# Kernel optimization log

Hardware: AMD Instinct MI355X
Metric: run time of the kernel (lower is better)

## Reference

```python
import jax, jax.numpy as jnp
import numpy as np

N = 50000      # nodes
K = 15         # k_max candidate neighbors per node
D = 128        # node_dim
H = 64         # hidden_dim
K_MIN = 2.0
K_MAX = 15.0
TAU = 0.5      # edge_tau
LAM = 1.0      # selector_lambda


def setup_inputs() -> dict:
    key = jax.random.key(0)
    ks = jax.random.split(key, 16)
    x = jax.random.normal(ks[0], (N, D), dtype=jnp.float32)
    src = jax.random.randint(ks[1], (N * K,), 0, N)
    dst = jnp.repeat(jnp.arange(N), K)  # edges grouped by dst, as the module requires
    edge_index = jnp.stack([src, dst]).astype(jnp.int64)
    edge_dist = jax.random.uniform(ks[2], (N * K,), dtype=jnp.float32)

    def lin(k, fin, fout):
        return jax.random.normal(k, (fin, fout), dtype=jnp.float32) / np.sqrt(fin)

    EIN = 2 * D + 1  # edge MLP input: [x_dst, x_src, dist]
    return {
        "x": x, "edge_index": edge_index, "edge_dist": edge_dist,
        "ew1": lin(ks[3], EIN, H), "eb1": jnp.zeros((H,), jnp.float32),
        "ew2": lin(ks[4], H, H),   "eb2": jnp.zeros((H,), jnp.float32),
        "ew3": lin(ks[5], H, 1),   "eb3": jnp.zeros((1,), jnp.float32),
        "dw1": lin(ks[6], D + 1, H), "db1": jnp.zeros((H,), jnp.float32),
        "dw2": lin(ks[7], H, H),     "db2": jnp.zeros((H,), jnp.float32),
        "dw3": lin(ks[8], H, 1),     "db3": jnp.zeros((1,), jnp.float32),
    }


def reference(x, edge_index, edge_dist, ew1, eb1, ew2, eb2, ew3, eb3,
              dw1, db1, dw2, db2, dw3, db3):
    src_mat = edge_index[0].reshape(N, K)              # (N, K)
    x_src = x[src_mat]                                 # gather: (N, K, D)
    x_dst = jnp.broadcast_to(x[:, None, :], (N, K, D))
    edge_feat = jnp.concatenate([x_dst, x_src, edge_dist.reshape(N, K, 1)], axis=-1)

    # edge MLP -> logits (eval mode: no gumbel-logistic noise)
    h = jax.nn.relu(edge_feat @ ew1 + eb1)
    h = jax.nn.relu(h @ ew2 + eb2)
    edge_logits = (h @ ew3 + eb3)[..., 0]              # (N, K)
    edge_energy = jax.nn.sigmoid(edge_logits / TAU)

    # degree MLP -> continuous k per node
    degree_hint = edge_energy.sum(axis=1, keepdims=True)
    g = jax.nn.relu(jnp.concatenate([x, degree_hint], axis=1) @ dw1 + db1)
    g = jax.nn.relu(g @ dw2 + db2)
    k_raw = (g @ dw3 + db3)[:, 0]
    k_cont = K_MIN + (K_MAX - K_MIN) * jax.nn.sigmoid(k_raw)  # (N,)

    # per-node descending sort + straight-through top-k gate
    perm = jnp.argsort(-edge_energy, axis=1)
    energy_sorted = jnp.take_along_axis(edge_energy, perm, axis=1)
    ranks = jnp.arange(1, K + 1, dtype=x.dtype)[None, :]
    gate_soft = jax.nn.sigmoid((k_cont[:, None] - ranks) / LAM)
    k_int = jnp.clip(jnp.round(k_cont), K_MIN, K_MAX)
    gate_hard = (ranks <= k_int[:, None]).astype(gate_soft.dtype)
    gate = gate_soft + jax.lax.stop_gradient(gate_hard - gate_soft)

    gated_sorted = energy_sorted * gate
    inv_perm = jnp.argsort(perm, axis=1)               # undo the sort
    edge_gate = jnp.take_along_axis(gate, inv_perm, axis=1)
    edge_weight = jnp.take_along_axis(gated_sorted, inv_perm, axis=1)

    denom = jnp.maximum(edge_weight.sum(axis=1, keepdims=True), 1e-12)
    edge_weight = edge_weight / denom
    return (edge_weight.reshape(-1), edge_gate.reshape(-1),
            edge_energy.reshape(-1), k_cont)
```

## Files before the change

kernel.cpp:

```cpp
#include <hip/hip_runtime.h>
#include <cmath>

#define NN 50000
#define KK 15
#define DD 128
#define HH 64
#define NKE (NN * KK)
#define TOFF ((size_t)DD * NN)
#define WS_NEED ((TOFF + 3 * (size_t)NN * HH) * 4)

__global__ __launch_bounds__(256) void kT(const float* __restrict__ x,
                                          float* __restrict__ xT) {
    __shared__ float s[64][DD + 1];
    int t = threadIdx.x;
    int r0 = blockIdx.x * 64;
#pragma unroll
    for (int i = 0; i < 8; ++i) {
        int idx = i * 256 + t;
        int rr = idx >> 5, cc = idx & 31;
        if (r0 + rr < NN) {
            float4 v = *(const float4*)(x + (size_t)(r0 + rr) * DD + cc * 4);
            s[rr][cc * 4 + 0] = v.x; s[rr][cc * 4 + 1] = v.y;
            s[rr][cc * 4 + 2] = v.z; s[rr][cc * 4 + 3] = v.w;
        }
    }
    __syncthreads();
    int lane = t & 63, wq = t >> 6;
    int n = r0 + lane;
    if (n >= NN) return;
#pragma unroll
    for (int i = 0; i < 32; ++i) {
        int k = i * 4 + wq;
        xT[(size_t)k * NN + n] = s[lane][k];
    }
}

__global__ __launch_bounds__(128, 4) void kP2(const float* __restrict__ xT,
                                              const float* __restrict__ ew1,
                                              const float* __restrict__ dw1,
                                              float* __restrict__ xabc) {
    int seg = blockIdx.y;
    const float* W = (seg == 0) ? ew1 : (seg == 1) ? (ew1 + DD * HH) : dw1;
    float* o = xabc + (size_t)seg * NN * HH;
    int n = blockIdx.x * 128 + threadIdx.x;
    if (n >= NN) return;

    float acc[HH];
#pragma unroll
    for (int j = 0; j < HH; ++j) acc[j] = 0.f;

#pragma unroll 1
    for (int k4 = 0; k4 < DD / 4; ++k4) {
        float x0 = xT[(size_t)(k4 * 4 + 0) * NN + n];
        float x1 = xT[(size_t)(k4 * 4 + 1) * NN + n];
        float x2 = xT[(size_t)(k4 * 4 + 2) * NN + n];
        float x3 = xT[(size_t)(k4 * 4 + 3) * NN + n];
        float xv[4] = {x0, x1, x2, x3};
#pragma unroll
        for (int m = 0; m < 4; ++m) {
            const float* wr = W + (k4 * 4 + m) * HH;
#pragma unroll
            for (int j4 = 0; j4 < 16; ++j4) {
                float4 w = *(const float4*)(wr + j4 * 4);
                acc[j4 * 4 + 0] = fmaf(xv[m], w.x, acc[j4 * 4 + 0]);
                acc[j4 * 4 + 1] = fmaf(xv[m], w.y, acc[j4 * 4 + 1]);
                acc[j4 * 4 + 2] = fmaf(xv[m], w.z, acc[j4 * 4 + 2]);
                acc[j4 * 4 + 3] = fmaf(xv[m], w.w, acc[j4 * 4 + 3]);
            }
        }
    }
    float* orow = o + (size_t)n * HH;
#pragma unroll
    for (int j4 = 0; j4 < 16; ++j4) {
        float4 v;
        v.x = acc[j4 * 4 + 0]; v.y = acc[j4 * 4 + 1];
        v.z = acc[j4 * 4 + 2]; v.w = acc[j4 * 4 + 3];
        *(float4*)(orow + j4 * 4) = v;
    }
}

__global__ __launch_bounds__(256, 4) void kP_fb(const float* __restrict__ x,
                                                const float* __restrict__ ew1,
                                                const float* __restrict__ dw1,
                                                float* __restrict__ xabc) {
    int lane = threadIdx.x & 63;
    int wv = threadIdx.x >> 6;
    int r0 = blockIdx.x * 32 + wv * 8;
    if (r0 >= NN) return;
    const float* W0 = ew1;
    const float* W1 = ew1 + DD * HH;
    const float* W2 = dw1;
    const float* xw = x + (size_t)r0 * DD;
    float a0[8], a1[8], a2[8];
#pragma unroll
    for (int r = 0; r < 8; ++r) { a0[r] = 0.f; a1[r] = 0.f; a2[r] = 0.f; }
#pragma unroll 1
    for (int i4 = 0; i4 < DD / 4; ++i4) {
        float w00 = W0[(i4 * 4 + 0) * HH + lane];
        float w01 = W0[(i4 * 4 + 1) * HH + lane];
        float w02 = W0[(i4 * 4 + 2) * HH + lane];
        float w03 = W0[(i4 * 4 + 3) * HH + lane];
        float w10 = W1[(i4 * 4 + 0) * HH + lane];
        float w11 = W1[(i4 * 4 + 1) * HH + lane];
        float w12 = W1[(i4 * 4 + 2) * HH + lane];
        float w13 = W1[(i4 * 4 + 3) * HH + lane];
        float w20 = W2[(i4 * 4 + 0) * HH + lane];
        float w21 = W2[(i4 * 4 + 1) * HH + lane];
        float w22 = W2[(i4 * 4 + 2) * HH + lane];
        float w23 = W2[(i4 * 4 + 3) * HH + lane];
#pragma unroll
        for (int r = 0; r < 8; ++r) {
            float4 xv = *(const float4*)(xw + r * DD + i4 * 4);
            a0[r] = fmaf(xv.x, w00, a0[r]); a0[r] = fmaf(xv.y, w01, a0[r]);
            a0[r] = fmaf(xv.z, w02, a0[r]); a0[r] = fmaf(xv.w, w03, a0[r]);
            a1[r] = fmaf(xv.x, w10, a1[r]); a1[r] = fmaf(xv.y, w11, a1[r]);
            a1[r] = fmaf(xv.z, w12, a1[r]); a1[r] = fmaf(xv.w, w13, a1[r]);
            a2[r] = fmaf(xv.x, w20, a2[r]); a2[r] = fmaf(xv.y, w21, a2[r]);
            a2[r] = fmaf(xv.z, w22, a2[r]); a2[r] = fmaf(xv.w, w23, a2[r]);
        }
    }
    float* o0 = xabc + (size_t)r0 * HH + lane;
    float* o1 = xabc + (size_t)NN * HH + (size_t)r0 * HH + lane;
    float* o2 = xabc + 2 * (size_t)NN * HH + (size_t)r0 * HH + lane;
#pragma unroll
    for (int r = 0; r < 8; ++r) {
        o0[r * HH] = a0[r]; o1[r * HH] = a1[r]; o2[r * HH] = a2[r];
    }
}

__global__ __launch_bounds__(128, 4) void kE(const int* __restrict__ srcIdx,
                                             const float* __restrict__ dist,
                                             const float* __restrict__ xabc,
                                             const float* __restrict__ ew1,
                                             const float* __restrict__ eb1,
                                             const float* __restrict__ ew2,
                                             const float* __restrict__ eb2,
                                             const float* __restrict__ ew3,
                                             const float* __restrict__ eb3,
                                             float* __restrict__ energy_out) {
    int e = blockIdx.x * 128 + threadIdx.x;
    if (e >= NKE) return;
    int s = srcIdx[e];
    int d = e / KK;
    float dd = dist[e];
    const float* A = xabc + (size_t)d * HH;
    const float* B = xabc + (size_t)NN * HH + (size_t)s * HH;
    const float* w1l = ew1 + 2 * DD * HH;

    float acc[HH];
#pragma unroll
    for (int j = 0; j < HH; ++j) acc[j] = 0.f;

    float4 a4 = *(const float4*)A;
    float4 bp0 = *(const float4*)B;
    float4 bp1 = *(const float4*)(B + 4);
#pragma unroll 1
    for (int i4 = 0; i4 < HH / 4; ++i4) {
        float4 a = a4, b = bp0;
        int n1 = (i4 + 1 < 16) ? (i4 + 1) : 15;
        int n2 = (i4 + 2 < 16) ? (i4 + 2) : 15;
        a4 = *(const float4*)(A + n1 * 4);
        bp0 = bp1;
        bp1 = *(const float4*)(B + n2 * 4);
        float h[4];
        h[0] = fmaxf(a.x + b.x + dd * w1l[i4 * 4 + 0] + eb1[i4 * 4 + 0], 0.f);
        h[1] = fmaxf(a.y + b.y + dd * w1l[i4 * 4 + 1] + eb1[i4 * 4 + 1], 0.f);
        h[2] = fmaxf(a.z + b.z + dd * w1l[i4 * 4 + 2] + eb1[i4 * 4 + 2], 0.f);
        h[3] = fmaxf(a.w + b.w + dd * w1l[i4 * 4 + 3] + eb1[i4 * 4 + 3], 0.f);
#pragma unroll
        for (int k = 0; k < 4; ++k) {
            const float* wr = ew2 + (i4 * 4 + k) * HH;
#pragma unroll
            for (int j4 = 0; j4 < 16; ++j4) {
                float4 w = *(const float4*)(wr + j4 * 4);
                acc[j4 * 4 + 0] = fmaf(h[k], w.x, acc[j4 * 4 + 0]);
                acc[j4 * 4 + 1] = fmaf(h[k], w.y, acc[j4 * 4 + 1]);
                acc[j4 * 4 + 2] = fmaf(h[k], w.z, acc[j4 * 4 + 2]);
                acc[j4 * 4 + 3] = fmaf(h[k], w.w, acc[j4 * 4 + 3]);
            }
        }
    }
    float lg = eb3[0];
#pragma unroll
    for (int j = 0; j < HH; ++j)
        lg = fmaf(fmaxf(acc[j] + eb2[j], 0.f), ew3[j], lg);
    energy_out[e] = 1.f / (1.f + expf(-2.f * lg));
}

__global__ __launch_bounds__(128, 4) void kF(const float* __restrict__ xabc,
                                             const float* __restrict__ dw1,
                                             const float* __restrict__ db1,
                                             const float* __restrict__ dw2,
                                             const float* __restrict__ db2,
                                             const float* __restrict__ dw3,
                                             const float* __restrict__ db3,
                                             float* __restrict__ out) {
    int n = blockIdx.x * 128 + threadIdx.x;
    if (n >= NN) return;
    const float* energy = out + 2 * (size_t)NKE;

    float ev[KK];
    float dh = 0.f;
#pragma unroll
    for (int j = 0; j < KK; ++j) {
        ev[j] = energy[(size_t)n * KK + j];
        dh += ev[j];
    }

    const float* XC = xabc + 2 * (size_t)NN * HH + (size_t)n * HH;
    const float* w1l = dw1 + DD * HH;

    float acc[HH];
#pragma unroll
    for (int j = 0; j < HH; ++j) acc[j] = 0.f;

    float4 c4 = *(const float4*)XC;
#pragma unroll 1
    for (int i4 = 0; i4 < HH / 4; ++i4) {
        float4 c = c4;
        int nx = (i4 + 1 < 16) ? (i4 + 1) : 15;
        c4 = *(const float4*)(XC + nx * 4);
        float cv[4] = {c.x, c.y, c.z, c.w};
#pragma unroll
        for (int m = 0; m < 4; ++m) {
            int k = i4 * 4 + m;
            float g = fmaxf(cv[m] + dh * w1l[k] + db1[k], 0.f);
            const float* wr = dw2 + k * HH;
#pragma unroll
            for (int j4 = 0; j4 < 16; ++j4) {
                float4 w = *(const float4*)(wr + j4 * 4);
                acc[j4 * 4 + 0] = fmaf(g, w.x, acc[j4 * 4 + 0]);
                acc[j4 * 4 + 1] = fmaf(g, w.y, acc[j4 * 4 + 1]);
                acc[j4 * 4 + 2] = fmaf(g, w.z, acc[j4 * 4 + 2]);
                acc[j4 * 4 + 3] = fmaf(g, w.w, acc[j4 * 4 + 3]);
            }
        }
    }
    float kraw = db3[0];
#pragma unroll
    for (int j = 0; j < HH; ++j)
        kraw = fmaf(fmaxf(acc[j] + db2[j], 0.f), dw3[j], kraw);

    float kcont = 2.f + 13.f / (1.f + expf(-kraw));
    out[3 * (size_t)NKE + n] = kcont;

    float se[16];
    int si[16];
#pragma unroll
    for (int j = 0; j < KK; ++j) { se[j] = ev[j]; si[j] = j; }
    se[15] = -1.f; si[15] = 15;

#pragma unroll
    for (int p = 1; p < 16; p <<= 1) {
#pragma unroll
        for (int k = p; k >= 1; k >>= 1) {
#pragma unroll
            for (int j = k & (p - 1); j + k < 16; j += 2 * k) {
#pragma unroll
                for (int i = 0; i < k; ++i) {
                    int a = i + j, b = i + j + k;
                    if (b < 16 && (a / (2 * p)) == (b / (2 * p))) {
                        bool sw = (se[b] > se[a]) ||
                                  (se[b] == se[a] && si[b] < si[a]);
                        float ea = sw ? se[b] : se[a];
                        float eb = sw ? se[a] : se[b];
                        int ia = sw ? si[b] : si[a];
                        int ib = sw ? si[a] : si[b];
                        se[a] = ea; se[b] = eb; si[a] = ia; si[b] = ib;
                    }
                }
            }
        }
    }

    float kint = rintf(kcont);
    kint = fminf(fmaxf(kint, 2.f), 15.f);

    float wsrt[KK];
    float denom = 0.f;
#pragma unroll
    for (int r = 0; r < KK; ++r) {
        float sel = ((float)(r + 1) <= kint) ? 1.f : 0.f;
        float wvv = se[r] * sel;
        wsrt[r] = wvv;
        denom += wvv;
    }
    denom = fmaxf(denom, 1e-12f);

#pragma unroll
    for (int r = 0; r < KK; ++r) {
        float sel = ((float)(r + 1) <= kint) ? 1.f : 0.f;
        int j0 = si[r];
        out[(size_t)NKE + (size_t)n * KK + j0] = sel;
        out[(size_t)n * KK + j0] = wsrt[r] / denom;
    }
}

extern "C" void kernel_launch(void* const* d_in, const int* in_sizes, int n_in,
                              void* d_out, int out_size, void* d_ws, size_t ws_size,
                              hipStream_t stream) {
    const float* x   = (const float*)d_in[0];
    const int*   ei  = (const int*)d_in[1];
    const float* ed  = (const float*)d_in[2];
    const float* ew1 = (const float*)d_in[3];
    const float* eb1 = (const float*)d_in[4];
    const float* ew2 = (const float*)d_in[5];
    const float* eb2 = (const float*)d_in[6];
    const float* ew3 = (const float*)d_in[7];
    const float* eb3 = (const float*)d_in[8];
    const float* dw1 = (const float*)d_in[9];
    const float* db1 = (const float*)d_in[10];
    const float* dw2 = (const float*)d_in[11];
    const float* db2 = (const float*)d_in[12];
    const float* dw3 = (const float*)d_in[13];
    const float* db3 = (const float*)d_in[14];
    float* out = (float*)d_out;
    float* ws  = (float*)d_ws;

    bool big = (ws_size >= WS_NEED);
    float* xabc = big ? (ws + TOFF) : ws;

    if (big) {
        hipLaunchKernelGGL(kT, dim3((NN + 63) / 64), dim3(256), 0, stream, x, ws);
        hipLaunchKernelGGL(kP2, dim3((NN + 127) / 128, 3), dim3(128), 0, stream,
                           ws, ew1, dw1, xabc);
    } else {
        hipLaunchKernelGGL(kP_fb, dim3((NN + 31) / 32), dim3(256), 0, stream,
                           x, ew1, dw1, xabc);
    }
    hipLaunchKernelGGL(kE, dim3((NKE + 127) / 128), dim3(128), 0, stream,
                       ei, ed, xabc, ew1, eb1, ew2, eb2, ew3, eb3,
                       out + 2 * (size_t)NKE);
    hipLaunchKernelGGL(kF, dim3((NN + 127) / 128), dim3(128), 0, stream,
                       xabc, dw1, db1, dw2, db2, dw3, db3, out);
}
```

Baseline: 326.9 us.

## Fuse edge MLP with degree MLP and split K across threads in projection

The edge-energy kernel and the per-node degree/sort kernel are merged into one kernel with 960-thread blocks. Each block handles 64 nodes' edges, keeps the energies in shared memory, and then lets 64 threads run the degree MLP, sort and gating. The projection kernel now splits the 128-long reduction across two thread halves and combines the partial sums in shared memory, doubling the threads available. This saves a launch and the energy re-read, but the node phase runs only one wavefront per large block, leaving most of that block idle. The 960-thread blocks with launch_bounds(960,4) may also force register spills for the 64-float accumulators.

```diff
diff --git a/kernel.cpp b/kernel.cpp
--- a/kernel.cpp
+++ b/kernel.cpp
@@ -35,47 +35,233 @@
     }
 }
 
-__global__ __launch_bounds__(128, 4) void kP2(const float* __restrict__ xT,
+__global__ __launch_bounds__(256, 4) void kP4(const float* __restrict__ xT,
                                               const float* __restrict__ ew1,
                                               const float* __restrict__ dw1,
                                               float* __restrict__ xabc) {
+    __shared__ float comb[HH * 128];
     int seg = blockIdx.y;
     const float* W = (seg == 0) ? ew1 : (seg == 1) ? (ew1 + DD * HH) : dw1;
-    float* o = xabc + (size_t)seg * NN * HH;
-    int n = blockIdx.x * 128 + threadIdx.x;
+    int t = threadIdx.x;
+    int nloc = t & 127;
+    int kh = t >> 7;
+    int n = blockIdx.x * 128 + nloc;
+    bool active = (n < NN);
+
+    float acc[HH];
+#pragma unroll
+    for (int j = 0; j < HH; ++j) acc[j] = 0.f;
+
+    if (active) {
+#pragma unroll 1
+        for (int k4 = kh * 16; k4 < kh * 16 + 16; ++k4) {
+            float x0 = xT[(size_t)(k4 * 4 + 0) * NN + n];
+            float x1 = xT[(size_t)(k4 * 4 + 1) * NN + n];
+            float x2 = xT[(size_t)(k4 * 4 + 2) * NN + n];
+            float x3 = xT[(size_t)(k4 * 4 + 3) * NN + n];
+            float xv[4] = {x0, x1, x2, x3};
+#pragma unroll
+            for (int m = 0; m < 4; ++m) {
+                const float* wr = W + (k4 * 4 + m) * HH;
+#pragma unroll
+                for (int j4 = 0; j4 < 16; ++j4) {
+                    float4 w = *(const float4*)(wr + j4 * 4);
+                    acc[j4 * 4 + 0] = fmaf(xv[m], w.x, acc[j4 * 4 + 0]);
+                    acc[j4 * 4 + 1] = fmaf(xv[m], w.y, acc[j4 * 4 + 1]);
+                    acc[j4 * 4 + 2] = fmaf(xv[m], w.z, acc[j4 * 4 + 2]);
+                    acc[j4 * 4 + 3] = fmaf(xv[m], w.w, acc[j4 * 4 + 3]);
+                }
+            }
+        }
+    }
+    if (kh == 1) {
+#pragma unroll
+        for (int j = 0; j < HH; ++j) comb[j * 128 + nloc] = acc[j];
+    }
+    __syncthreads();
+    if (kh == 0 && active) {
+#pragma unroll
+        for (int j = 0; j < HH; ++j) acc[j] += comb[j * 128 + nloc];
+        float* orow = xabc + (size_t)seg * NN * HH + (size_t)n * HH;
+#pragma unroll
+        for (int j4 = 0; j4 < 16; ++j4) {
+            float4 v;
+            v.x = acc[j4 * 4 + 0]; v.y = acc[j4 * 4 + 1];
+            v.z = acc[j4 * 4 + 2]; v.w = acc[j4 * 4 + 3];
+            *(float4*)(orow + j4 * 4) = v;
+        }
+    }
+}
+
+__global__ __launch_bounds__(960, 4) void kEF(const int* __restrict__ srcIdx,
+                                              const float* __restrict__ dist,
+                                              const float* __restrict__ xabc,
+                                              const float* __restrict__ ew1,
+                                              const float* __restrict__ eb1,
+                                              const float* __restrict__ ew2,
+                                              const float* __restrict__ eb2,
+                                              const float* __restrict__ ew3,
+                                              const float* __restrict__ eb3,
+                                              const float* __restrict__ dw1,
+                                              const float* __restrict__ db1,
+                                              const float* __restrict__ dw2,
+                                              const float* __restrict__ db2,
+                                              const float* __restrict__ dw3,
+                                              const float* __restrict__ db3,
+                                              float* __restrict__ out) {
+    __shared__ float ebuf[960];
+    int e = blockIdx.x * 960 + threadIdx.x;
+    float* energy_out = out + 2 * (size_t)NKE;
+
+    if (e < NKE) {
+        int s = srcIdx[e];
+        int d = e / KK;
+        float dd = dist[e];
+        const float* A = xabc + (size_t)d * HH;
+        const float* B = xabc + (size_t)NN * HH + (size_t)s * HH;
+        const float* w1l = ew1 + 2 * DD * HH;
+
+        float acc[HH];
+#pragma unroll
+        for (int j = 0; j < HH; ++j) acc[j] = 0.f;
+
+        float4 a4 = *(const float4*)A;
+        float4 bp0 = *(const float4*)B;
+        float4 bp1 = *(const float4*)(B + 4);
+#pragma unroll 1
+        for (int i4 = 0; i4 < HH / 4; ++i4) {
+            float4 a = a4, b = bp0;
+            int n1 = (i4 + 1 < 16) ? (i4 + 1) : 15;
+            int n2 = (i4 + 2 < 16) ? (i4 + 2) : 15;
+            a4 = *(const float4*)(A + n1 * 4);
+            bp0 = bp1;
+            bp1 = *(const float4*)(B + n2 * 4);
+            float h[4];
+            h[0] = fmaxf(a.x + b.x + dd * w1l[i4 * 4 + 0] + eb1[i4 * 4 + 0], 0.f);
+            h[1] = fmaxf(a.y + b.y + dd * w1l[i4 * 4 + 1] + eb1[i4 * 4 + 1], 0.f);
+            h[2] = fmaxf(a.z + b.z + dd * w1l[i4 * 4 + 2] + eb1[i4 * 4 + 2], 0.f);
+            h[3] = fmaxf(a.w + b.w + dd * w1l[i4 * 4 + 3] + eb1[i4 * 4 + 3], 0.f);
+#pragma unroll
+            for (int k = 0; k < 4; ++k) {
+                const float* wr = ew2 + (i4 * 4 + k) * HH;
+#pragma unroll
+                for (int j4 = 0; j4 < 16; ++j4) {
+                    float4 w = *(const float4*)(wr + j4 * 4);
+                    acc[j4 * 4 + 0] = fmaf(h[k], w.x, acc[j4 * 4 + 0]);
+                    acc[j4 * 4 + 1] = fmaf(h[k], w.y, acc[j4 * 4 + 1]);
+                    acc[j4 * 4 + 2] = fmaf(h[k], w.z, acc[j4 * 4 + 2]);
+                    acc[j4 * 4 + 3] = fmaf(h[k], w.w, acc[j4 * 4 + 3]);
+                }
+            }
+        }
+        float lg = eb3[0];
+#pragma unroll
+        for (int j = 0; j < HH; ++j)
+            lg = fmaf(fmaxf(acc[j] + eb2[j], 0.f), ew3[j], lg);
+        float en = 1.f / (1.f + expf(-2.f * lg));
+        energy_out[e] = en;
+        ebuf[threadIdx.x] = en;
+    }
+    __syncthreads();
+
+    if (threadIdx.x >= 64) return;
+    int n = blockIdx.x * 64 + (int)threadIdx.x;
     if (n >= NN) return;
 
+    float ev[KK];
+    float dh = 0.f;
+#pragma unroll
+    for (int j = 0; j < KK; ++j) {
+        ev[j] = ebuf[threadIdx.x * KK + j];
+        dh += ev[j];
+    }
+
+    const float* XC = xabc + 2 * (size_t)NN * HH + (size_t)n * HH;
+    const float* w1l = dw1 + DD * HH;
+
     float acc[HH];
 #pragma unroll
     for (int j = 0; j < HH; ++j) acc[j] = 0.f;
 
+    float4 c4 = *(const float4*)XC;
 #pragma unroll 1
-    for (int k4 = 0; k4 < DD / 4; ++k4) {
-        float x0 = xT[(size_t)(k4 * 4 + 0) * NN + n];
-        float x1 = xT[(size_t)(k4 * 4 + 1) * NN + n];
-        float x2 = xT[(size_t)(k4 * 4 + 2) * NN + n];
-        float x3 = xT[(size_t)(k4 * 4 + 3) * NN + n];
-        float xv[4] = {x0, x1, x2, x3};
+    for (int i4 = 0; i4 < HH / 4; ++i4) {
+        float4 c = c4;
+        int nx = (i4 + 1 < 16) ? (i4 + 1) : 15;
+        c4 = *(const float4*)(XC + nx * 4);
+        float cv[4] = {c.x, c.y, c.z, c.w};
 #pragma unroll
         for (int m = 0; m < 4; ++m) {
-            const float* wr = W + (k4 * 4 + m) * HH;
+            int k = i4 * 4 + m;
+            float g = fmaxf(cv[m] + dh * w1l[k] + db1[k], 0.f);
+            const float* wr = dw2 + k * HH;
 #pragma unroll
             for (int j4 = 0; j4 < 16; ++j4) {
                 float4 w = *(const float4*)(wr + j4 * 4);
-                acc[j4 * 4 + 0] = fmaf(xv[m], w.x, acc[j4 * 4 + 0]);
-                acc[j4 * 4 + 1] = fmaf(xv[m], w.y, acc[j4 * 4 + 1]);
-                acc[j4 * 4 + 2] = fmaf(xv[m], w.z, acc[j4 * 4 + 2]);
-                acc[j4 * 4 + 3] = fmaf(xv[m], w.w, acc[j4 * 4 + 3]);
+                acc[j4 * 4 + 0] = fmaf(g, w.x, acc[j4 * 4 + 0]);
+                acc[j4 * 4 + 1] = fmaf(g, w.y, acc[j4 * 4 + 1]);
+                acc[j4 * 4 + 2] = fmaf(g, w.z, acc[j4 * 4 + 2]);
+                acc[j4 * 4 + 3] = fmaf(g, w.w, acc[j4 * 4 + 3]);
             }
         }
     }
-    float* orow = o + (size_t)n * HH;
-#pragma unroll
-    for (int j4 = 0; j4 < 16; ++j4) {
-        float4 v;
-        v.x = acc[j4 * 4 + 0]; v.y = acc[j4 * 4 + 1];
-        v.z = acc[j4 * 4 + 2]; v.w = acc[j4 * 4 + 3];
-        *(float4*)(orow + j4 * 4) = v;
+    float kraw = db3[0];
+#pragma unroll
+    for (int j = 0; j < HH; ++j)
+        kraw = fmaf(fmaxf(acc[j] + db2[j], 0.f), dw3[j], kraw);
+
+    float kcont = 2.f + 13.f / (1.f + expf(-kraw));
+    out[3 * (size_t)NKE + n] = kcont;
+
+    float se[16];
+    int si[16];
+#pragma unroll
+    for (int j = 0; j < KK; ++j) { se[j] = ev[j]; si[j] = j; }
+    se[15] = -1.f; si[15] = 15;
+
+#pragma unroll
+    for (int p = 1; p < 16; p <<= 1) {
+#pragma unroll
+        for (int k = p; k >= 1; k >>= 1) {
+#pragma unroll
+            for (int j = k & (p - 1); j + k < 16; j += 2 * k) {
+#pragma unroll
+                for (int i = 0; i < k; ++i) {
+                    int a = i + j, b = i + j + k;
+                    if (b < 16 && (a / (2 * p)) == (b / (2 * p))) {
+                        bool sw = (se[b] > se[a]) ||
+                                  (se[b] == se[a] && si[b] < si[a]);
+                        float ea = sw ? se[b] : se[a];
+                        float eb = sw ? se[a] : se[b];
+                        int ia = sw ? si[b] : si[a];
+                        int ib = sw ? si[a] : si[b];
+                        se[a] = ea; se[b] = eb; si[a] = ia; si[b] = ib;
+                    }
+                }
+            }
+        }
+    }
+
+    float kint = rintf(kcont);
+    kint = fminf(fmaxf(kint, 2.f), 15.f);
+
+    float wsrt[KK];
+    float denom = 0.f;
+#pragma unroll
+    for (int r = 0; r < KK; ++r) {
+        float sel = ((float)(r + 1) <= kint) ? 1.f : 0.f;
+        float wvv = se[r] * sel;
+        wsrt[r] = wvv;
+        denom += wvv;
+    }
+    denom = fmaxf(denom, 1e-12f);
+
+#pragma unroll
+    for (int r = 0; r < KK; ++r) {
+        float sel = ((float)(r + 1) <= kint) ? 1.f : 0.f;
+        int j0 = si[r];
+        out[(size_t)NKE + (size_t)n * KK + j0] = sel;
+        out[(size_t)n * KK + j0] = wsrt[r] / denom;
     }
 }
 
@@ -125,174 +311,6 @@
 #pragma unroll
     for (int r = 0; r < 8; ++r) {
         o0[r * HH] = a0[r]; o1[r * HH] = a1[r]; o2[r * HH] = a2[r];
-    }
-}
-
-__global__ __launch_bounds__(128, 4) void kE(const int* __restrict__ srcIdx,
-                                             const float* __restrict__ dist,
-                                             const float* __restrict__ xabc,
-                                             const float* __restrict__ ew1,
-                                             const float* __restrict__ eb1,
-                                             const float* __restrict__ ew2,
-                                             const float* __restrict__ eb2,
-                                             const float* __restrict__ ew3,
-                                             const float* __restrict__ eb3,
-                                             float* __restrict__ energy_out) {
-    int e = blockIdx.x * 128 + threadIdx.x;
-    if (e >= NKE) return;
-    int s = srcIdx[e];
-    int d = e / KK;
-    float dd = dist[e];
-    const float* A = xabc + (size_t)d * HH;
-    const float* B = xabc + (size_t)NN * HH + (size_t)s * HH;
-    const float* w1l = ew1 + 2 * DD * HH;
-
-    float acc[HH];
-#pragma unroll
-    for (int j = 0; j < HH; ++j) acc[j] = 0.f;
-
-    float4 a4 = *(const float4*)A;
-    float4 bp0 = *(const float4*)B;
-    float4 bp1 = *(const float4*)(B + 4);
-#pragma unroll 1
-    for (int i4 = 0; i4 < HH / 4; ++i4) {
-        float4 a = a4, b = bp0;
-        int n1 = (i4 + 1 < 16) ? (i4 + 1) : 15;
-        int n2 = (i4 + 2 < 16) ? (i4 + 2) : 15;
-        a4 = *(const float4*)(A + n1 * 4);
-        bp0 = bp1;
-        bp1 = *(const float4*)(B + n2 * 4);
-        float h[4];
-        h[0] = fmaxf(a.x + b.x + dd * w1l[i4 * 4 + 0] + eb1[i4 * 4 + 0], 0.f);
-        h[1] = fmaxf(a.y + b.y + dd * w1l[i4 * 4 + 1] + eb1[i4 * 4 + 1], 0.f);
-        h[2] = fmaxf(a.z + b.z + dd * w1l[i4 * 4 + 2] + eb1[i4 * 4 + 2], 0.f);
-        h[3] = fmaxf(a.w + b.w + dd * w1l[i4 * 4 + 3] + eb1[i4 * 4 + 3], 0.f);
-#pragma unroll
-        for (int k = 0; k < 4; ++k) {
-            const float* wr = ew2 + (i4 * 4 + k) * HH;
-#pragma unroll
-            for (int j4 = 0; j4 < 16; ++j4) {
-                float4 w = *(const float4*)(wr + j4 * 4);
-                acc[j4 * 4 + 0] = fmaf(h[k], w.x, acc[j4 * 4 + 0]);
-                acc[j4 * 4 + 1] = fmaf(h[k], w.y, acc[j4 * 4 + 1]);
-                acc[j4 * 4 + 2] = fmaf(h[k], w.z, acc[j4 * 4 + 2]);
-                acc[j4 * 4 + 3] = fmaf(h[k], w.w, acc[j4 * 4 + 3]);
-            }
-        }
-    }
-    float lg = eb3[0];
-#pragma unroll
-    for (int j = 0; j < HH; ++j)
-        lg = fmaf(fmaxf(acc[j] + eb2[j], 0.f), ew3[j], lg);
-    energy_out[e] = 1.f / (1.f + expf(-2.f * lg));
-}
-
-__global__ __launch_bounds__(128, 4) void kF(const float* __restrict__ xabc,
-                                             const float* __restrict__ dw1,
-                                             const float* __restrict__ db1,
-                                             const float* __restrict__ dw2,
-                                             const float* __restrict__ db2,
-                                             const float* __restrict__ dw3,
-                                             const float* __restrict__ db3,
-                                             float* __restrict__ out) {
-    int n = blockIdx.x * 128 + threadIdx.x;
-    if (n >= NN) return;
-    const float* energy = out + 2 * (size_t)NKE;
-
-    float ev[KK];
-    float dh = 0.f;
-#pragma unroll
-    for (int j = 0; j < KK; ++j) {
-        ev[j] = energy[(size_t)n * KK + j];
-        dh += ev[j];
-    }
-
-    const float* XC = xabc + 2 * (size_t)NN * HH + (size_t)n * HH;
-    const float* w1l = dw1 + DD * HH;
-
-    float acc[HH];
-#pragma unroll
-    for (int j = 0; j < HH; ++j) acc[j] = 0.f;
-
-    float4 c4 = *(const float4*)XC;
-#pragma unroll 1
-    for (int i4 = 0; i4 < HH / 4; ++i4) {
-        float4 c = c4;
-        int nx = (i4 + 1 < 16) ? (i4 + 1) : 15;
-        c4 = *(const float4*)(XC + nx * 4);
-        float cv[4] = {c.x, c.y, c.z, c.w};
-#pragma unroll
-        for (int m = 0; m < 4; ++m) {
-            int k = i4 * 4 + m;
-            float g = fmaxf(cv[m] + dh * w1l[k] + db1[k], 0.f);
-            const float* wr = dw2 + k * HH;
-#pragma unroll
-            for (int j4 = 0; j4 < 16; ++j4) {
-                float4 w = *(const float4*)(wr + j4 * 4);
-                acc[j4 * 4 + 0] = fmaf(g, w.x, acc[j4 * 4 + 0]);
-                acc[j4 * 4 + 1] = fmaf(g, w.y, acc[j4 * 4 + 1]);
-                acc[j4 * 4 + 2] = fmaf(g, w.z, acc[j4 * 4 + 2]);
-                acc[j4 * 4 + 3] = fmaf(g, w.w, acc[j4 * 4 + 3]);
-            }
-        }
-    }
-    float kraw = db3[0];
-#pragma unroll
-    for (int j = 0; j < HH; ++j)
-        kraw = fmaf(fmaxf(acc[j] + db2[j], 0.f), dw3[j], kraw);
-
-    float kcont = 2.f + 13.f / (1.f + expf(-kraw));
-    out[3 * (size_t)NKE + n] = kcont;
-
-    float se[16];
-    int si[16];
-#pragma unroll
-    for (int j = 0; j < KK; ++j) { se[j] = ev[j]; si[j] = j; }
-    se[15] = -1.f; si[15] = 15;
-
-#pragma unroll
-    for (int p = 1; p < 16; p <<= 1) {
-#pragma unroll
-        for (int k = p; k >= 1; k >>= 1) {
-#pragma unroll
-            for (int j = k & (p - 1); j + k < 16; j += 2 * k) {
-#pragma unroll
-                for (int i = 0; i < k; ++i) {
-                    int a = i + j, b = i + j + k;
-                    if (b < 16 && (a / (2 * p)) == (b / (2 * p))) {
-                        bool sw = (se[b] > se[a]) ||
-                                  (se[b] == se[a] && si[b] < si[a]);
-                        float ea = sw ? se[b] : se[a];
-                        float eb = sw ? se[a] : se[b];
-                        int ia = sw ? si[b] : si[a];
-                        int ib = sw ? si[a] : si[b];
-                        se[a] = ea; se[b] = eb; si[a] = ia; si[b] = ib;
-                    }
-                }
-            }
-        }
-    }
-
-    float kint = rintf(kcont);
-    kint = fminf(fmaxf(kint, 2.f), 15.f);
-
-    float wsrt[KK];
-    float denom = 0.f;
-#pragma unroll
-    for (int r = 0; r < KK; ++r) {
-        float sel = ((float)(r + 1) <= kint) ? 1.f : 0.f;
-        float wvv = se[r] * sel;
-        wsrt[r] = wvv;
-        denom += wvv;
-    }
-    denom = fmaxf(denom, 1e-12f);
-
-#pragma unroll
-    for (int r = 0; r < KK; ++r) {
-        float sel = ((float)(r + 1) <= kint) ? 1.f : 0.f;
-        int j0 = si[r];
-        out[(size_t)NKE + (size_t)n * KK + j0] = sel;
-        out[(size_t)n * KK + j0] = wsrt[r] / denom;
     }
 }
 
@@ -322,15 +340,13 @@
 
     if (big) {
         hipLaunchKernelGGL(kT, dim3((NN + 63) / 64), dim3(256), 0, stream, x, ws);
-        hipLaunchKernelGGL(kP2, dim3((NN + 127) / 128, 3), dim3(128), 0, stream,
+        hipLaunchKernelGGL(kP4, dim3((NN + 127) / 128, 3), dim3(256), 0, stream,
                            ws, ew1, dw1, xabc);
     } else {
         hipLaunchKernelGGL(kP_fb, dim3((NN + 31) / 32), dim3(256), 0, stream,
                            x, ew1, dw1, xabc);
     }
-    hipLaunchKernelGGL(kE, dim3((NKE + 127) / 128), dim3(128), 0, stream,
+    hipLaunchKernelGGL(kEF, dim3((NKE + 959) / 960), dim3(960), 0, stream,
                        ei, ed, xabc, ew1, eb1, ew2, eb2, ew3, eb3,
-                       out + 2 * (size_t)NKE);
-    hipLaunchKernelGGL(kF, dim3((NN + 127) / 128), dim3(128), 0, stream,
-                       xabc, dw1, db1, dw2, db2, dw3, db3, out);
-}
+                       dw1, db1, dw2, db2, dw3, db3, out);
+}
```

New measurement: 531.2 us. 1.62x slower.

## Fuse edge and degree MLP kernels; split projection over output quarters

Applied to the files above, without the earlier changes.

The edge-energy kernel and the per-node degree/sort kernel are merged into one kernel. Each 256-thread block computes 240 edge energies (16 nodes), stages them in shared memory, then 16 threads run the degree MLP, sort and gate for those nodes. This removes a launch and the re-read of energies from global memory. The cost is that 240 threads sit idle during the node phase, which has a 64-wide serial MLP per thread. The projection kernel is also split into 12 y-blocks, each computing 16 output columns with 256 threads. That lowers register pressure and raises occupancy, but it re-reads the transposed x four times.

```diff
diff --git a/kernel.cpp b/kernel.cpp
--- a/kernel.cpp
+++ b/kernel.cpp
@@ -35,47 +35,226 @@
     }
 }
 
-__global__ __launch_bounds__(128, 4) void kP2(const float* __restrict__ xT,
+__global__ __launch_bounds__(256, 8) void kP6(const float* __restrict__ xT,
                                               const float* __restrict__ ew1,
                                               const float* __restrict__ dw1,
                                               float* __restrict__ xabc) {
-    int seg = blockIdx.y;
-    const float* W = (seg == 0) ? ew1 : (seg == 1) ? (ew1 + DD * HH) : dw1;
-    float* o = xabc + (size_t)seg * NN * HH;
-    int n = blockIdx.x * 128 + threadIdx.x;
+    int n = blockIdx.x * 256 + threadIdx.x;
     if (n >= NN) return;
-
-    float acc[HH];
-#pragma unroll
-    for (int j = 0; j < HH; ++j) acc[j] = 0.f;
+    int seg = blockIdx.y >> 2;
+    int jq  = blockIdx.y & 3;
+    const float* W = ((seg == 0) ? ew1 : (seg == 1) ? (ew1 + DD * HH) : dw1)
+                     + jq * 16;
+
+    float acc[16];
+#pragma unroll
+    for (int j = 0; j < 16; ++j) acc[j] = 0.f;
 
 #pragma unroll 1
     for (int k4 = 0; k4 < DD / 4; ++k4) {
-        float x0 = xT[(size_t)(k4 * 4 + 0) * NN + n];
-        float x1 = xT[(size_t)(k4 * 4 + 1) * NN + n];
-        float x2 = xT[(size_t)(k4 * 4 + 2) * NN + n];
-        float x3 = xT[(size_t)(k4 * 4 + 3) * NN + n];
-        float xv[4] = {x0, x1, x2, x3};
+        float xk[4];
+#pragma unroll
+        for (int m = 0; m < 4; ++m)
+            xk[m] = xT[(size_t)(k4 * 4 + m) * NN + n];
+        float4 w[4][4];
 #pragma unroll
         for (int m = 0; m < 4; ++m) {
             const float* wr = W + (k4 * 4 + m) * HH;
+            w[m][0] = *(const float4*)(wr + 0);
+            w[m][1] = *(const float4*)(wr + 4);
+            w[m][2] = *(const float4*)(wr + 8);
+            w[m][3] = *(const float4*)(wr + 12);
+        }
+#pragma unroll
+        for (int m = 0; m < 4; ++m) {
+#pragma unroll
+            for (int q = 0; q < 4; ++q) {
+                acc[q * 4 + 0] = fmaf(xk[m], w[m][q].x, acc[q * 4 + 0]);
+                acc[q * 4 + 1] = fmaf(xk[m], w[m][q].y, acc[q * 4 + 1]);
+                acc[q * 4 + 2] = fmaf(xk[m], w[m][q].z, acc[q * 4 + 2]);
+                acc[q * 4 + 3] = fmaf(xk[m], w[m][q].w, acc[q * 4 + 3]);
+            }
+        }
+    }
+    float* o = xabc + (size_t)seg * NN * HH + (size_t)n * HH + jq * 16;
+#pragma unroll
+    for (int q = 0; q < 4; ++q) {
+        float4 v;
+        v.x = acc[q * 4 + 0]; v.y = acc[q * 4 + 1];
+        v.z = acc[q * 4 + 2]; v.w = acc[q * 4 + 3];
+        *(float4*)(o + q * 4) = v;
+    }
+}
+
+__global__ __launch_bounds__(256, 4) void kEF2(const int* __restrict__ srcIdx,
+                                               const float* __restrict__ dist,
+                                               const float* __restrict__ xabc,
+                                               const float* __restrict__ ew1,
+                                               const float* __restrict__ eb1,
+                                               const float* __restrict__ ew2,
+                                               const float* __restrict__ eb2,
+                                               const float* __restrict__ ew3,
+                                               const float* __restrict__ eb3,
+                                               const float* __restrict__ dw1,
+                                               const float* __restrict__ db1,
+                                               const float* __restrict__ dw2,
+                                               const float* __restrict__ db2,
+                                               const float* __restrict__ dw3,
+                                               const float* __restrict__ db3,
+                                               float* __restrict__ out) {
+    __shared__ float ebuf[240];
+    int tid = threadIdx.x;
+    float* energy_out = out + 2 * (size_t)NKE;
+
+    if (tid < 240) {
+        int e = blockIdx.x * 240 + tid;
+        int s = srcIdx[e];
+        int d = e / KK;
+        float dd = dist[e];
+        const float* A = xabc + (size_t)d * HH;
+        const float* B = xabc + (size_t)NN * HH + (size_t)s * HH;
+        const float* w1l = ew1 + 2 * DD * HH;
+
+        float acc[HH];
+#pragma unroll
+        for (int j = 0; j < HH; ++j) acc[j] = 0.f;
+
+        float4 a4 = *(const float4*)A;
+        float4 bp0 = *(const float4*)B;
+        float4 bp1 = *(const float4*)(B + 4);
+#pragma unroll 1
+        for (int i4 = 0; i4 < HH / 4; ++i4) {
+            float4 a = a4, b = bp0;
+            int n1 = (i4 + 1 < 16) ? (i4 + 1) : 15;
+            int n2 = (i4 + 2 < 16) ? (i4 + 2) : 15;
+            a4 = *(const float4*)(A + n1 * 4);
+            bp0 = bp1;
+            bp1 = *(const float4*)(B + n2 * 4);
+            float h[4];
+            h[0] = fmaxf(a.x + b.x + dd * w1l[i4 * 4 + 0] + eb1[i4 * 4 + 0], 0.f);
+            h[1] = fmaxf(a.y + b.y + dd * w1l[i4 * 4 + 1] + eb1[i4 * 4 + 1], 0.f);
+            h[2] = fmaxf(a.z + b.z + dd * w1l[i4 * 4 + 2] + eb1[i4 * 4 + 2], 0.f);
+            h[3] = fmaxf(a.w + b.w + dd * w1l[i4 * 4 + 3] + eb1[i4 * 4 + 3], 0.f);
+#pragma unroll
+            for (int k = 0; k < 4; ++k) {
+                const float* wr = ew2 + (i4 * 4 + k) * HH;
+#pragma unroll
+                for (int j4 = 0; j4 < 16; ++j4) {
+                    float4 w = *(const float4*)(wr + j4 * 4);
+                    acc[j4 * 4 + 0] = fmaf(h[k], w.x, acc[j4 * 4 + 0]);
+                    acc[j4 * 4 + 1] = fmaf(h[k], w.y, acc[j4 * 4 + 1]);
+                    acc[j4 * 4 + 2] = fmaf(h[k], w.z, acc[j4 * 4 + 2]);
+                    acc[j4 * 4 + 3] = fmaf(h[k], w.w, acc[j4 * 4 + 3]);
+                }
+            }
+        }
+        float lg = eb3[0];
+#pragma unroll
+        for (int j = 0; j < HH; ++j)
+            lg = fmaf(fmaxf(acc[j] + eb2[j], 0.f), ew3[j], lg);
+        float en = 1.f / (1.f + expf(-2.f * lg));
+        energy_out[e] = en;
+        ebuf[tid] = en;
+    }
+    __syncthreads();
+
+    if (tid >= 16) return;
+    int n = blockIdx.x * 16 + tid;
+
+    float ev[KK];
+    float dh = 0.f;
+#pragma unroll
+    for (int j = 0; j < KK; ++j) {
+        ev[j] = ebuf[tid * KK + j];
+        dh += ev[j];
+    }
+
+    const float* XC = xabc + 2 * (size_t)NN * HH + (size_t)n * HH;
+    const float* w1l = dw1 + DD * HH;
+
+    float acc[HH];
+#pragma unroll
+    for (int j = 0; j < HH; ++j) acc[j] = 0.f;
+
+    float4 c4 = *(const float4*)XC;
+#pragma unroll 1
+    for (int i4 = 0; i4 < HH / 4; ++i4) {
+        float4 c = c4;
+        int nx = (i4 + 1 < 16) ? (i4 + 1) : 15;
+        c4 = *(const float4*)(XC + nx * 4);
+        float cv[4] = {c.x, c.y, c.z, c.w};
+#pragma unroll
+        for (int m = 0; m < 4; ++m) {
+            int k = i4 * 4 + m;
+            float g = fmaxf(cv[m] + dh * w1l[k] + db1[k], 0.f);
+            const float* wr = dw2 + k * HH;
 #pragma unroll
             for (int j4 = 0; j4 < 16; ++j4) {
                 float4 w = *(const float4*)(wr + j4 * 4);
-                acc[j4 * 4 + 0] = fmaf(xv[m], w.x, acc[j4 * 4 + 0]);
-                acc[j4 * 4 + 1] = fmaf(xv[m], w.y, acc[j4 * 4 + 1]);
-                acc[j4 * 4 + 2] = fmaf(xv[m], w.z, acc[j4 * 4 + 2]);
-                acc[j4 * 4 + 3] = fmaf(xv[m], w.w, acc[j4 * 4 + 3]);
+                acc[j4 * 4 + 0] = fmaf(g, w.x, acc[j4 * 4 + 0]);
+                acc[j4 * 4 + 1] = fmaf(g, w.y, acc[j4 * 4 + 1]);
+                acc[j4 * 4 + 2] = fmaf(g, w.z, acc[j4 * 4 + 2]);
+                acc[j4 * 4 + 3] = fmaf(g, w.w, acc[j4 * 4 + 3]);
             }
         }
     }
-    float* orow = o + (size_t)n * HH;
-#pragma unroll
-    for (int j4 = 0; j4 < 16; ++j4) {
-        float4 v;
-        v.x = acc[j4 * 4 + 0]; v.y = acc[j4 * 4 + 1];
-        v.z = acc[j4 * 4 + 2]; v.w = acc[j4 * 4 + 3];
-        *(float4*)(orow + j4 * 4) = v;
+    float kraw = db3[0];
+#pragma unroll
+    for (int j = 0; j < HH; ++j)
+        kraw = fmaf(fmaxf(acc[j] + db2[j], 0.f), dw3[j], kraw);
+
+    float kcont = 2.f + 13.f / (1.f + expf(-kraw));
+    out[3 * (size_t)NKE + n] = kcont;
+
+    float se[16];
+    int si[16];
+#pragma unroll
+    for (int j = 0; j < KK; ++j) { se[j] = ev[j]; si[j] = j; }
+    se[15] = -1.f; si[15] = 15;
+
+#pragma unroll
+    for (int p = 1; p < 16; p <<= 1) {
+#pragma unroll
+        for (int k = p; k >= 1; k >>= 1) {
+#pragma unroll
+            for (int j = k & (p - 1); j + k < 16; j += 2 * k) {
+#pragma unroll
+                for (int i = 0; i < k; ++i) {
+                    int a = i + j, b = i + j + k;
+                    if (b < 16 && (a / (2 * p)) == (b / (2 * p))) {
+                        bool sw = (se[b] > se[a]) ||
+                                  (se[b] == se[a] && si[b] < si[a]);
+                        float ea = sw ? se[b] : se[a];
+                        float eb = sw ? se[a] : se[b];
+                        int ia = sw ? si[b] : si[a];
+                        int ib = sw ? si[a] : si[b];
+                        se[a] = ea; se[b] = eb; si[a] = ia; si[b] = ib;
+                    }
+                }
+            }
+        }
+    }
+
+    float kint = rintf(kcont);
+    kint = fminf(fmaxf(kint, 2.f), 15.f);
+
+    float wsrt[KK];
+    float denom = 0.f;
+#pragma unroll
+    for (int r = 0; r < KK; ++r) {
+        float sel = ((float)(r + 1) <= kint) ? 1.f : 0.f;
+        float wvv = se[r] * sel;
+        wsrt[r] = wvv;
+        denom += wvv;
+    }
+    denom = fmaxf(denom, 1e-12f);
+
+#pragma unroll
+    for (int r = 0; r < KK; ++r) {
+        float sel = ((float)(r + 1) <= kint) ? 1.f : 0.f;
+        int j0 = si[r];
+        out[(size_t)NKE + (size_t)n * KK + j0] = sel;
+        out[(size_t)n * KK + j0] = wsrt[r] / denom;
     }
 }
 
@@ -125,174 +304,6 @@
 #pragma unroll
     for (int r = 0; r < 8; ++r) {
         o0[r * HH] = a0[r]; o1[r * HH] = a1[r]; o2[r * HH] = a2[r];
-    }
-}
-
-__global__ __launch_bounds__(128, 4) void kE(const int* __restrict__ srcIdx,
-                                             const float* __restrict__ dist,
-                                             const float* __restrict__ xabc,
-                                             const float* __restrict__ ew1,
-                                             const float* __restrict__ eb1,
-                                             const float* __restrict__ ew2,
-                                             const float* __restrict__ eb2,
-                                             const float* __restrict__ ew3,
-                                             const float* __restrict__ eb3,
-                                             float* __restrict__ energy_out) {
-    int e = blockIdx.x * 128 + threadIdx.x;
-    if (e >= NKE) return;
-    int s = srcIdx[e];
-    int d = e / KK;
-    float dd = dist[e];
-    const float* A = xabc + (size_t)d * HH;
-    const float* B = xabc + (size_t)NN * HH + (size_t)s * HH;
-    const float* w1l = ew1 + 2 * DD * HH;
-
-    float acc[HH];
-#pragma unroll
-    for (int j = 0; j < HH; ++j) acc[j] = 0.f;
-
-    float4 a4 = *(const float4*)A;
-    float4 bp0 = *(const float4*)B;
-    float4 bp1 = *(const float4*)(B + 4);
-#pragma unroll 1
-    for (int i4 = 0; i4 < HH / 4; ++i4) {
-        float4 a = a4, b = bp0;
-        int n1 = (i4 + 1 < 16) ? (i4 + 1) : 15;
-        int n2 = (i4 + 2 < 16) ? (i4 + 2) : 15;
-        a4 = *(const float4*)(A + n1 * 4);
-        bp0 = bp1;
-        bp1 = *(const float4*)(B + n2 * 4);
-        float h[4];
-        h[0] = fmaxf(a.x + b.x + dd * w1l[i4 * 4 + 0] + eb1[i4 * 4 + 0], 0.f);
-        h[1] = fmaxf(a.y + b.y + dd * w1l[i4 * 4 + 1] + eb1[i4 * 4 + 1], 0.f);
-        h[2] = fmaxf(a.z + b.z + dd * w1l[i4 * 4 + 2] + eb1[i4 * 4 + 2], 0.f);
-        h[3] = fmaxf(a.w + b.w + dd * w1l[i4 * 4 + 3] + eb1[i4 * 4 + 3], 0.f);
-#pragma unroll
-        for (int k = 0; k < 4; ++k) {
-            const float* wr = ew2 + (i4 * 4 + k) * HH;
-#pragma unroll
-            for (int j4 = 0; j4 < 16; ++j4) {
-                float4 w = *(const float4*)(wr + j4 * 4);
-                acc[j4 * 4 + 0] = fmaf(h[k], w.x, acc[j4 * 4 + 0]);
-                acc[j4 * 4 + 1] = fmaf(h[k], w.y, acc[j4 * 4 + 1]);
-                acc[j4 * 4 + 2] = fmaf(h[k], w.z, acc[j4 * 4 + 2]);
-                acc[j4 * 4 + 3] = fmaf(h[k], w.w, acc[j4 * 4 + 3]);
-            }
-        }
-    }
-    float lg = eb3[0];
-#pragma unroll
-    for (int j = 0; j < HH; ++j)
-        lg = fmaf(fmaxf(acc[j] + eb2[j], 0.f), ew3[j], lg);
-    energy_out[e] = 1.f / (1.f + expf(-2.f * lg));
-}
-
-__global__ __launch_bounds__(128, 4) void kF(const float* __restrict__ xabc,
-                                             const float* __restrict__ dw1,
-                                             const float* __restrict__ db1,
-                                             const float* __restrict__ dw2,
-                                             const float* __restrict__ db2,
-                                             const float* __restrict__ dw3,
-                                             const float* __restrict__ db3,
-                                             float* __restrict__ out) {
-    int n = blockIdx.x * 128 + threadIdx.x;
-    if (n >= NN) return;
-    const float* energy = out + 2 * (size_t)NKE;
-
-    float ev[KK];
-    float dh = 0.f;
-#pragma unroll
-    for (int j = 0; j < KK; ++j) {
-        ev[j] = energy[(size_t)n * KK + j];
-        dh += ev[j];
-    }
-
-    const float* XC = xabc + 2 * (size_t)NN * HH + (size_t)n * HH;
-    const float* w1l = dw1 + DD * HH;
-
-    float acc[HH];
-#pragma unroll
-    for (int j = 0; j < HH; ++j) acc[j] = 0.f;
-
-    float4 c4 = *(const float4*)XC;
-#pragma unroll 1
-    for (int i4 = 0; i4 < HH / 4; ++i4) {
-        float4 c = c4;
-        int nx = (i4 + 1 < 16) ? (i4 + 1) : 15;
-        c4 = *(const float4*)(XC + nx * 4);
-        float cv[4] = {c.x, c.y, c.z, c.w};
-#pragma unroll
-        for (int m = 0; m < 4; ++m) {
-            int k = i4 * 4 + m;
-            float g = fmaxf(cv[m] + dh * w1l[k] + db1[k], 0.f);
-            const float* wr = dw2 + k * HH;
-#pragma unroll
-            for (int j4 = 0; j4 < 16; ++j4) {
-                float4 w = *(const float4*)(wr + j4 * 4);
-                acc[j4 * 4 + 0] = fmaf(g, w.x, acc[j4 * 4 + 0]);
-                acc[j4 * 4 + 1] = fmaf(g, w.y, acc[j4 * 4 + 1]);
-                acc[j4 * 4 + 2] = fmaf(g, w.z, acc[j4 * 4 + 2]);
-                acc[j4 * 4 + 3] = fmaf(g, w.w, acc[j4 * 4 + 3]);
-            }
-        }
-    }
-    float kraw = db3[0];
-#pragma unroll
-    for (int j = 0; j < HH; ++j)
-        kraw = fmaf(fmaxf(acc[j] + db2[j], 0.f), dw3[j], kraw);
-
-    float kcont = 2.f + 13.f / (1.f + expf(-kraw));
-    out[3 * (size_t)NKE + n] = kcont;
-
-    float se[16];
-    int si[16];
-#pragma unroll
-    for (int j = 0; j < KK; ++j) { se[j] = ev[j]; si[j] = j; }
-    se[15] = -1.f; si[15] = 15;
-
-#pragma unroll
-    for (int p = 1; p < 16; p <<= 1) {
-#pragma unroll
-        for (int k = p; k >= 1; k >>= 1) {
-#pragma unroll
-            for (int j = k & (p - 1); j + k < 16; j += 2 * k) {
-#pragma unroll
-                for (int i = 0; i < k; ++i) {
-                    int a = i + j, b = i + j + k;
-                    if (b < 16 && (a / (2 * p)) == (b / (2 * p))) {
-                        bool sw = (se[b] > se[a]) ||
-                                  (se[b] == se[a] && si[b] < si[a]);
-                        float ea = sw ? se[b] : se[a];
-                        float eb = sw ? se[a] : se[b];
-                        int ia = sw ? si[b] : si[a];
-                        int ib = sw ? si[a] : si[b];
-                        se[a] = ea; se[b] = eb; si[a] = ia; si[b] = ib;
-                    }
-                }
-            }
-        }
-    }
-
-    float kint = rintf(kcont);
-    kint = fminf(fmaxf(kint, 2.f), 15.f);
-
-    float wsrt[KK];
-    float denom = 0.f;
-#pragma unroll
-    for (int r = 0; r < KK; ++r) {
-        float sel = ((float)(r + 1) <= kint) ? 1.f : 0.f;
-        float wvv = se[r] * sel;
-        wsrt[r] = wvv;
-        denom += wvv;
-    }
-    denom = fmaxf(denom, 1e-12f);
-
-#pragma unroll
-    for (int r = 0; r < KK; ++r) {
-        float sel = ((float)(r + 1) <= kint) ? 1.f : 0.f;
-        int j0 = si[r];
-        out[(size_t)NKE + (size_t)n * KK + j0] = sel;
-        out[(size_t)n * KK + j0] = wsrt[r] / denom;
     }
 }
 
@@ -322,15 +333,13 @@
 
     if (big) {
         hipLaunchKernelGGL(kT, dim3((NN + 63) / 64), dim3(256), 0, stream, x, ws);
-        hipLaunchKernelGGL(kP2, dim3((NN + 127) / 128, 3), dim3(128), 0, stream,
+        hipLaunchKernelGGL(kP6, dim3((NN + 255) / 256, 12), dim3(256), 0, stream,
                            ws, ew1, dw1, xabc);
     } else {
         hipLaunchKernelGGL(kP_fb, dim3((NN + 31) / 32), dim3(256), 0, stream,
                            x, ew1, dw1, xabc);
     }
-    hipLaunchKernelGGL(kE, dim3((NKE + 127) / 128), dim3(128), 0, stream,
+    hipLaunchKernelGGL(kEF2, dim3(NKE / 240), dim3(256), 0, stream,
                        ei, ed, xabc, ew1, eb1, ew2, eb2, ew3, eb3,
-                       out + 2 * (size_t)NKE);
-    hipLaunchKernelGGL(kF, dim3((NN + 127) / 128), dim3(128), 0, stream,
-                       xabc, dw1, db1, dw2, db2, dw3, db3, out);
-}
+                       dw1, db1, dw2, db2, dw3, db3, out);
+}
```

Result: faster. 270.6 us (-17.2%).
